# Kernel optimization log

Hardware: AMD Instinct MI355X
Metric: run time of the kernel (lower is better)

The kernel has to match this reference:

```python
import jax, jax.numpy as jnp
import numpy as np

K = 3
PAD = 1
EPS = 1e-5


def _unfold(x, k, pad):
    # torch.nn.Unfold(k, dilation=1, padding=pad, stride=1): output [B, C*k*k, L]
    # with channel-major ordering (c, ki, kj) in the second dim.
    B, C, H, W = x.shape
    xp = jnp.pad(x, ((0, 0), (0, 0), (pad, pad), (pad, pad)))
    Ho = H + 2 * pad - k + 1
    Wo = W + 2 * pad - k + 1
    patches = jnp.stack(
        [xp[:, :, i:i + Ho, j:j + Wo] for i in range(k) for j in range(k)],
        axis=2,
    )  # [B, C, k*k, Ho, Wo]
    return patches.reshape(B, C * k * k, Ho * Wo)


def _conv1x1(x, w, b):
    return jnp.einsum('bchw,oc->bohw', x, w) + b[None, :, None, None]


def _bn(x, g, b):
    # training-mode BatchNorm2d: batch stats over (B,H,W), biased variance
    mu = x.mean(axis=(0, 2, 3), keepdims=True)
    var = x.var(axis=(0, 2, 3), keepdims=True)
    return (x - mu) * jax.lax.rsqrt(var + EPS) * g[None, :, None, None] + b[None, :, None, None]


def _tri(x, w, b, g, be):
    return jax.nn.relu(_bn(_conv1x1(x, w, b), g, be))


def reference(x, w1, b1, g1, be1, w2, b2, g2, be2, wf, bf, gf, bef):
    B, C, H, W = x.shape
    k2 = K * K
    c = k2 // 2
    tri1 = _tri(x, w1, b1, g1, be1)  # key map  [B,C,H,W] (m=1)
    tri2 = _tri(x, w2, b2, g2, be2)  # query map
    # NOTE: faithful to source: plain row-major reshape of [B, C*k2, L] -> [B, C, L, k2]
    ku = _unfold(tri1, K, PAD).reshape(B, C, -1, k2)
    qu = _unfold(tri2, K, PAD).reshape(B, C, -1, k2)
    logits = ku * qu[..., c:c + 1] + ku[..., c:c + 1] * qu
    dl_weight = jax.nn.softmax(logits, axis=-1)[:, None]  # [B,1,C,L,k2]
    xu = _unfold(x, K, PAD).reshape(B, 1, C, -1, k2)       # m=1 -> [B,1,C,L,k2]
    # NOTE: faithful to source: row-major reshape to [B, C, k2, L], sum over axis -2
    pre = (dl_weight * xu).reshape(B, C, k2, -1).sum(axis=-2).reshape(B, C, H, W)
    return jax.nn.relu(_bn(_conv1x1(pre, wf, bf), gf, bef))


def setup_inputs() -> dict:
    key = jax.random.key(0)
    B, C, O, H, W = 4, 256, 256, 64, 64
    ks = jax.random.split(key, 4)
    s = 1.0 / np.sqrt(C)
    return {
        'x': jax.random.normal(ks[0], (B, C, H, W), dtype=jnp.float32),
        'w1': jax.random.normal(ks[1], (C, C), dtype=jnp.float32) * s,
        'b1': jnp.zeros((C,), jnp.float32),
        'g1': jnp.ones((C,), jnp.float32),
        'be1': jnp.zeros((C,), jnp.float32),
        'w2': jax.random.normal(ks[2], (C, C), dtype=jnp.float32) * s,
        'b2': jnp.zeros((C,), jnp.float32),
        'g2': jnp.ones((C,), jnp.float32),
        'be2': jnp.zeros((C,), jnp.float32),
        'wf': jax.random.normal(ks[3], (O, C), dtype=jnp.float32) * s,
        'bf': jnp.zeros((O,), jnp.float32),
        'gf': jnp.ones((O,), jnp.float32),
        'bef': jnp.zeros((O,), jnp.float32),
    }
```

## Files before the change

### kernel.cpp

```cpp
#include <hip/hip_runtime.h>

#define L 4096
#define CCH 256
#define NB 4
#define KP 40

typedef __attribute__((ext_vector_type(8))) short short8;
typedef __attribute__((ext_vector_type(4))) float f32x4;
typedef unsigned short ushort_t;

__device__ __forceinline__ unsigned short f2bf(float f) {
    unsigned u = __builtin_bit_cast(unsigned, f);
    u += 0x7FFF + ((u >> 16) & 1);
    return (unsigned short)(u >> 16);
}
__device__ __forceinline__ float bflo(unsigned w) {
    return __builtin_bit_cast(float, w << 16);
}
__device__ __forceinline__ float bfhi(unsigned w) {
    return __builtin_bit_cast(float, w & 0xFFFF0000u);
}

__global__ __launch_bounds__(256, 2) void dual_gemm_k(
    const float* __restrict__ x,
    const float* __restrict__ w1, const float* __restrict__ b1,
    const float* __restrict__ w2, const float* __restrict__ b2,
    ushort_t* __restrict__ y1, ushort_t* __restrict__ y2)
{
    __shared__ short sA1[128 * KP];
    __shared__ short sA2[128 * KP];
    __shared__ short sB [64 * KP];

    const int tid = threadIdx.x;
    const int l0 = blockIdx.x * 64;
    const int o0 = blockIdx.y * 128;
    const int b  = blockIdx.z;

    const int wv = tid >> 6;
    const int lane = tid & 63;
    const int m = lane & 15;
    const int quad = lane >> 4;

    const float* xb = x + (size_t)b * CCH * L;

    const int sl = tid & 63, soct = tid >> 6;
    const int sr = tid & 127, sh = tid >> 7;

    f32x4 acc1[2][4], acc2[2][4];
    #pragma unroll
    for (int io = 0; io < 2; ++io)
        #pragma unroll
        for (int jl = 0; jl < 4; ++jl) {
            acc1[io][jl] = (f32x4){0.f,0.f,0.f,0.f};
            acc2[io][jl] = (f32x4){0.f,0.f,0.f,0.f};
        }

    for (int s = 0; s < 8; ++s) {
        const int k0 = s * 32;
        __syncthreads();
        {
            const float* xs = xb + (size_t)(k0 + soct * 8) * L + l0 + sl;
            short8 v;
            #pragma unroll
            for (int j = 0; j < 8; ++j) v[j] = (short)f2bf(xs[(size_t)j * L]);
            *(short8*)&sB[sl * KP + soct * 8] = v;
        }
        {
            const float4* wp = (const float4*)&w1[(size_t)(o0 + sr) * CCH + k0 + sh * 16];
            float4 c0 = wp[0], c1 = wp[1], c2 = wp[2], c3 = wp[3];
            short8 p0 = {(short)f2bf(c0.x),(short)f2bf(c0.y),(short)f2bf(c0.z),(short)f2bf(c0.w),
                         (short)f2bf(c1.x),(short)f2bf(c1.y),(short)f2bf(c1.z),(short)f2bf(c1.w)};
            short8 p1 = {(short)f2bf(c2.x),(short)f2bf(c2.y),(short)f2bf(c2.z),(short)f2bf(c2.w),
                         (short)f2bf(c3.x),(short)f2bf(c3.y),(short)f2bf(c3.z),(short)f2bf(c3.w)};
            *(short8*)&sA1[sr * KP + sh * 16]     = p0;
            *(short8*)&sA1[sr * KP + sh * 16 + 8] = p1;
            const float4* wq = (const float4*)&w2[(size_t)(o0 + sr) * CCH + k0 + sh * 16];
            float4 d0 = wq[0], d1 = wq[1], d2 = wq[2], d3 = wq[3];
            short8 q0 = {(short)f2bf(d0.x),(short)f2bf(d0.y),(short)f2bf(d0.z),(short)f2bf(d0.w),
                         (short)f2bf(d1.x),(short)f2bf(d1.y),(short)f2bf(d1.z),(short)f2bf(d1.w)};
            short8 q1 = {(short)f2bf(d2.x),(short)f2bf(d2.y),(short)f2bf(d2.z),(short)f2bf(d2.w),
                         (short)f2bf(d3.x),(short)f2bf(d3.y),(short)f2bf(d3.z),(short)f2bf(d3.w)};
            *(short8*)&sA2[sr * KP + sh * 16]     = q0;
            *(short8*)&sA2[sr * KP + sh * 16 + 8] = q1;
        }
        __syncthreads();
        short8 a1[2], a2[2], bf[4];
        #pragma unroll
        for (int io = 0; io < 2; ++io) {
            a1[io] = *(const short8*)&sA1[(wv * 32 + io * 16 + m) * KP + quad * 8];
            a2[io] = *(const short8*)&sA2[(wv * 32 + io * 16 + m) * KP + quad * 8];
        }
        #pragma unroll
        for (int jl = 0; jl < 4; ++jl)
            bf[jl] = *(const short8*)&sB[(jl * 16 + m) * KP + quad * 8];
        #pragma unroll
        for (int io = 0; io < 2; ++io)
            #pragma unroll
            for (int jl = 0; jl < 4; ++jl) {
                acc1[io][jl] = __builtin_amdgcn_mfma_f32_16x16x32_bf16(a1[io], bf[jl], acc1[io][jl], 0, 0, 0);
                acc2[io][jl] = __builtin_amdgcn_mfma_f32_16x16x32_bf16(a2[io], bf[jl], acc2[io][jl], 0, 0, 0);
            }
    }

    #pragma unroll
    for (int io = 0; io < 2; ++io)
        #pragma unroll
        for (int reg = 0; reg < 4; ++reg) {
            const int o = o0 + wv * 32 + io * 16 + quad * 4 + reg;
            const float bb1 = b1[o], bb2 = b2[o];
            const size_t ro = ((size_t)b * CCH + o) * L + l0 + m;
            #pragma unroll
            for (int jl = 0; jl < 4; ++jl) {
                y1[ro + jl * 16] = f2bf(acc1[io][jl][reg] + bb1);
                y2[ro + jl * 16] = f2bf(acc2[io][jl][reg] + bb2);
            }
        }
}

__global__ __launch_bounds__(256, 2) void single_gemm_k(
    const ushort_t* __restrict__ x,
    const float* __restrict__ w, const float* __restrict__ bb,
    ushort_t* __restrict__ y)
{
    __shared__ short sA[128 * KP];
    __shared__ short sB[64 * KP];

    const int tid = threadIdx.x;
    const int l0 = blockIdx.x * 64;
    const int o0 = blockIdx.y * 128;
    const int b  = blockIdx.z;

    const int wv = tid >> 6;
    const int lane = tid & 63;
    const int m = lane & 15;
    const int quad = lane >> 4;

    const ushort_t* xb = x + (size_t)b * CCH * L;

    const int sl = tid & 63, soct = tid >> 6;
    const int sr = tid & 127, sh = tid >> 7;

    f32x4 acc[2][4];
    #pragma unroll
    for (int io = 0; io < 2; ++io)
        #pragma unroll
        for (int jl = 0; jl < 4; ++jl)
            acc[io][jl] = (f32x4){0.f,0.f,0.f,0.f};

    for (int s = 0; s < 8; ++s) {
        const int k0 = s * 32;
        __syncthreads();
        {
            const ushort_t* xs = xb + (size_t)(k0 + soct * 8) * L + l0 + sl;
            short8 v;
            #pragma unroll
            for (int j = 0; j < 8; ++j) v[j] = (short)xs[(size_t)j * L];
            *(short8*)&sB[sl * KP + soct * 8] = v;
        }
        {
            const float4* wp = (const float4*)&w[(size_t)(o0 + sr) * CCH + k0 + sh * 16];
            float4 c0 = wp[0], c1 = wp[1], c2 = wp[2], c3 = wp[3];
            short8 p0 = {(short)f2bf(c0.x),(short)f2bf(c0.y),(short)f2bf(c0.z),(short)f2bf(c0.w),
                         (short)f2bf(c1.x),(short)f2bf(c1.y),(short)f2bf(c1.z),(short)f2bf(c1.w)};
            short8 p1 = {(short)f2bf(c2.x),(short)f2bf(c2.y),(short)f2bf(c2.z),(short)f2bf(c2.w),
                         (short)f2bf(c3.x),(short)f2bf(c3.y),(short)f2bf(c3.z),(short)f2bf(c3.w)};
            *(short8*)&sA[sr * KP + sh * 16]     = p0;
            *(short8*)&sA[sr * KP + sh * 16 + 8] = p1;
        }
        __syncthreads();
        short8 a[2], bf[4];
        #pragma unroll
        for (int io = 0; io < 2; ++io)
            a[io] = *(const short8*)&sA[(wv * 32 + io * 16 + m) * KP + quad * 8];
        #pragma unroll
        for (int jl = 0; jl < 4; ++jl)
            bf[jl] = *(const short8*)&sB[(jl * 16 + m) * KP + quad * 8];
        #pragma unroll
        for (int io = 0; io < 2; ++io)
            #pragma unroll
            for (int jl = 0; jl < 4; ++jl)
                acc[io][jl] = __builtin_amdgcn_mfma_f32_16x16x32_bf16(a[io], bf[jl], acc[io][jl], 0, 0, 0);
    }

    #pragma unroll
    for (int io = 0; io < 2; ++io)
        #pragma unroll
        for (int reg = 0; reg < 4; ++reg) {
            const int o = o0 + wv * 32 + io * 16 + quad * 4 + reg;
            const float b0 = bb[o];
            const size_t ro = ((size_t)b * CCH + o) * L + l0 + m;
            #pragma unroll
            for (int jl = 0; jl < 4; ++jl)
                y[ro + jl * 16] = f2bf(acc[io][jl][reg] + b0);
        }
}

__device__ __forceinline__ void bn_stats_body(
    const ushort_t* y, const float* gamma, const float* beta,
    float* scale, float* shift, int c, int tid)
{
    float s = 0.f, s2 = 0.f;
    for (int b = 0; b < NB; ++b) {
        const uint4* p = (const uint4*)(y + ((size_t)b * CCH + c) * L);
        #pragma unroll
        for (int r = 0; r < 2; ++r) {
            uint4 v = p[r * 256 + tid];
            unsigned w[4] = {v.x, v.y, v.z, v.w};
            #pragma unroll
            for (int u = 0; u < 4; ++u) {
                float a = bflo(w[u]), bb = bfhi(w[u]);
                s  += a + bb;
                s2 += a * a + bb * bb;
            }
        }
    }
    #pragma unroll
    for (int off = 32; off > 0; off >>= 1) {
        s  += __shfl_down(s, off);
        s2 += __shfl_down(s2, off);
    }
    __shared__ float red[2][4];
    if ((tid & 63) == 0) { red[0][tid >> 6] = s; red[1][tid >> 6] = s2; }
    __syncthreads();
    if (tid == 0) {
        float S  = red[0][0] + red[0][1] + red[0][2] + red[0][3];
        float S2 = red[1][0] + red[1][1] + red[1][2] + red[1][3];
        const float invN = 1.f / (NB * (float)L);
        float mean = S * invN;
        float var  = S2 * invN - mean * mean;
        float rstd = rsqrtf(var + 1e-5f);
        float g = gamma[c];
        scale[c] = g * rstd;
        shift[c] = beta[c] - mean * g * rstd;
    }
}

__global__ __launch_bounds__(256) void bn_stats_k(
    const ushort_t* __restrict__ y, const float* __restrict__ gamma,
    const float* __restrict__ beta,
    float* __restrict__ scale, float* __restrict__ shift)
{
    bn_stats_body(y, gamma, beta, scale, shift, blockIdx.x, threadIdx.x);
}

__global__ __launch_bounds__(256) void bn_stats2_k(
    const ushort_t* __restrict__ y1, const float* __restrict__ g1, const float* __restrict__ be1,
    float* __restrict__ sc1, float* __restrict__ sh1,
    const ushort_t* __restrict__ y2, const float* __restrict__ g2, const float* __restrict__ be2,
    float* __restrict__ sc2, float* __restrict__ sh2)
{
    const int c = blockIdx.x & 255;
    if (blockIdx.x < 256) bn_stats_body(y1, g1, be1, sc1, sh1, c, threadIdx.x);
    else                  bn_stats_body(y2, g2, be2, sc2, sh2, c, threadIdx.x);
}

__global__ __launch_bounds__(512, 4) void attention_k(
    const float* __restrict__ x,
    const ushort_t* __restrict__ y1,
    const ushort_t* __restrict__ y2,
    const float* __restrict__ s1sc, const float* __restrict__ s1sh,
    const float* __restrict__ s2sc, const float* __restrict__ s2sh,
    ushort_t* __restrict__ pre)
{
    __shared__ unsigned sKQ[L];
    __shared__ float    sXv[L];
    __shared__ uint2    sCI[L];

    const int bc = blockIdx.x;
    const int tid = threadIdx.x;
    const int ch = bc & 255;
    const size_t off = (size_t)bc * L;

    const float sc1 = s1sc[ch], sh1 = s1sh[ch];
    const float sc2 = s2sc[ch], sh2 = s2sh[ch];

    const float4* x4 = (const float4*)(x + off);

    {
        uint4 ak = ((const uint4*)(y1 + off))[tid];
        uint4 aq = ((const uint4*)(y2 + off))[tid];
        unsigned wks[4] = {ak.x, ak.y, ak.z, ak.w};
        unsigned wqs[4] = {aq.x, aq.y, aq.z, aq.w};
        #pragma unroll
        for (int u = 0; u < 4; ++u) {
            float klo = fmaxf(fmaf(bflo(wks[u]), sc1, sh1), 0.f);
            float khi = fmaxf(fmaf(bfhi(wks[u]), sc1, sh1), 0.f);
            float qlo = fmaxf(fmaf(bflo(wqs[u]), sc2, sh2), 0.f);
            float qhi = fmaxf(fmaf(bfhi(wqs[u]), sc2, sh2), 0.f);
            sKQ[8 * tid + 2 * u]     = (unsigned)f2bf(klo) | ((unsigned)f2bf(qlo) << 16);
            sKQ[8 * tid + 2 * u + 1] = (unsigned)f2bf(khi) | ((unsigned)f2bf(qhi) << 16);
        }
        ((float4*)sXv)[2 * tid]     = x4[2 * tid];
        ((float4*)sXv)[2 * tid + 1] = x4[2 * tid + 1];
    }
    __syncthreads();

    #pragma unroll
    for (int r = 0; r < 8; ++r) {
        const int lp = r * 512 + tid;
        const int base = 9 * lp;
        float kv[9], qv[9];
        unsigned cw = 0;
        #pragma unroll
        for (int j = 0; j < 9; ++j) {
            int f = base + j;
            int t = f >> 12;
            int l = f & 4095;
            int di = (t * 86) >> 8;
            int dj = t - di * 3;
            int ii = (l >> 6) + di - 1;
            int jj = (l & 63) + dj - 1;
            bool ok = ((unsigned)ii < 64u) && ((unsigned)jj < 64u);
            int src = ((ii << 6) + jj) & 4095;
            unsigned w = sKQ[src];
            w = ok ? w : 0u;
            if (j == 4) cw = w;
            kv[j] = bflo(w);
            qv[j] = bfhi(w);
        }
        const float kc = kv[4], qc = qv[4];
        float s01 = __expf(kv[0] * qc + kc * qv[0]) + __expf(kv[1] * qc + kc * qv[1]);
        float s23 = __expf(kv[2] * qc + kc * qv[2]) + __expf(kv[3] * qc + kc * qv[3]);
        float s45 = __expf(kv[4] * qc + kc * qv[4]) + __expf(kv[5] * qc + kc * qv[5]);
        float s67 = __expf(kv[6] * qc + kc * qv[6]) + __expf(kv[7] * qc + kc * qv[7]);
        float s = ((s01 + s23) + (s45 + s67)) + __expf(kv[8] * qc + kc * qv[8]);
        uint2 ci;
        ci.x = cw;
        ci.y = __builtin_bit_cast(unsigned, -__logf(s));
        sCI[lp] = ci;
    }
    __syncthreads();

    #pragma unroll
    for (int r = 0; r < 8; ++r) {
        const int l = r * 512 + tid;
        const int li = l >> 6, lj = l & 63;
        float acc = 0.f;
        #pragma unroll
        for (int t = 0; t < 9; ++t) {
            const int f = (t << 12) + l;
            const unsigned lp = (unsigned)f / 9u;
            uint2 ci = sCI[lp];
            const float kc = bflo(ci.x), qc = bfhi(ci.x);
            const float cn = __builtin_bit_cast(float, ci.y);
            const int di = t / 3, dj = t % 3;
            int ii = li + di - 1;
            int jj = lj + dj - 1;
            bool ok = ((unsigned)ii < 64u) && ((unsigned)jj < 64u);
            int src = ((ii << 6) + jj) & 4095;
            unsigned w = sKQ[src];
            float xj = sXv[src];
            w  = ok ? w : 0u;
            xj = ok ? xj : 0.f;
            const float kj = bflo(w), qj = bfhi(w);
            float e = __expf(fmaf(kj, qc, fmaf(kc, qj, cn)));
            acc = fmaf(e, xj, acc);
        }
        pre[off + l] = f2bf(acc);
    }
}

__global__ __launch_bounds__(256) void bn_apply_k(
    const ushort_t* __restrict__ yf,
    const float* __restrict__ scale, const float* __restrict__ shift,
    float* __restrict__ out)
{
    const int i = blockIdx.x * 256 + threadIdx.x;
    const int ch = (i >> 9) & 255;
    const float sc = scale[ch], sh = shift[ch];

    uint4 v = ((const uint4*)yf)[i];
    unsigned w[4] = {v.x, v.y, v.z, v.w};
    float4 o0, o1;
    o0.x = fmaxf(fmaf(bflo(w[0]), sc, sh), 0.f);
    o0.y = fmaxf(fmaf(bfhi(w[0]), sc, sh), 0.f);
    o0.z = fmaxf(fmaf(bflo(w[1]), sc, sh), 0.f);
    o0.w = fmaxf(fmaf(bfhi(w[1]), sc, sh), 0.f);
    o1.x = fmaxf(fmaf(bflo(w[2]), sc, sh), 0.f);
    o1.y = fmaxf(fmaf(bfhi(w[2]), sc, sh), 0.f);
    o1.z = fmaxf(fmaf(bflo(w[3]), sc, sh), 0.f);
    o1.w = fmaxf(fmaf(bfhi(w[3]), sc, sh), 0.f);
    ((float4*)out)[2 * i]     = o0;
    ((float4*)out)[2 * i + 1] = o1;
}

extern "C" void kernel_launch(void* const* d_in, const int* in_sizes, int n_in,
                              void* d_out, int out_size, void* d_ws, size_t ws_size,
                              hipStream_t stream) {
    const float* x   = (const float*)d_in[0];
    const float* w1  = (const float*)d_in[1];
    const float* b1  = (const float*)d_in[2];
    const float* g1  = (const float*)d_in[3];
    const float* be1 = (const float*)d_in[4];
    const float* w2  = (const float*)d_in[5];
    const float* b2  = (const float*)d_in[6];
    const float* g2  = (const float*)d_in[7];
    const float* be2 = (const float*)d_in[8];
    const float* wf  = (const float*)d_in[9];
    const float* bf  = (const float*)d_in[10];
    const float* gf  = (const float*)d_in[11];
    const float* bef = (const float*)d_in[12];
    float* out = (float*)d_out;

    const size_t NEL = (size_t)NB * CCH * L;
    ushort_t* y1b = (ushort_t*)d_ws;
    ushort_t* y2b = y1b + NEL;
    float* st = (float*)(y2b + NEL);
    float* s1sc = st,        *s1sh = st + 256;
    float* s2sc = st + 512,  *s2sh = st + 768;
    float* sfsc = st + 1024, *sfsh = st + 1280;

    dim3 gg(64, 2, 4);
    dual_gemm_k<<<gg, 256, 0, stream>>>(x, w1, b1, w2, b2, y1b, y2b);
    bn_stats2_k<<<512, 256, 0, stream>>>(y1b, g1, be1, s1sc, s1sh,
                                         y2b, g2, be2, s2sc, s2sh);
    attention_k<<<NB * CCH, 512, 0, stream>>>(x, y1b, y2b,
                                              s1sc, s1sh, s2sc, s2sh,
                                              y2b);
    single_gemm_k<<<gg, 256, 0, stream>>>(y2b, wf, bf, y1b);
    bn_stats_k<<<256, 256, 0, stream>>>(y1b, gf, bef, sfsc, sfsh);
    bn_apply_k<<<(int)(NEL / 2048), 256, 0, stream>>>(y1b, sfsc, sfsh, out);
}
```

Measured before the change: 180.9 us.

## Use zero-padded shared tiles and bf16 x in attention kernel

The attention kernel now stores the key/query map and x in shared arrays with zero guard rows before and after the image. This removes per-tap row bounds checks and leaves only column-edge masks. x is stored as bf16 instead of fp32, which halves its LDS footprint and adds a rounding step to x. The first pass now reads contiguous 9-element runs with a specialized fast path. The second pass interchanges loops so each tap's offsets are computed once across eight accumulators. These changes aim to cut integer index arithmetic, LDS usage and predication, at the cost of extra precision loss on x.

```diff
diff --git a/kernel.cpp b/kernel.cpp
--- a/kernel.cpp
+++ b/kernel.cpp
@@ -4,6 +4,7 @@
 #define CCH 256
 #define NB 4
 #define KP 40
+#define GOF 72
 
 typedef __attribute__((ext_vector_type(8))) short short8;
 typedef __attribute__((ext_vector_type(4))) float f32x4;
@@ -19,6 +20,9 @@
 }
 __device__ __forceinline__ float bfhi(unsigned w) {
     return __builtin_bit_cast(float, w & 0xFFFF0000u);
+}
+__device__ __forceinline__ float bfu(ushort_t h) {
+    return __builtin_bit_cast(float, (unsigned)h << 16);
 }
 
 __global__ __launch_bounds__(256, 2) void dual_gemm_k(
@@ -262,9 +266,9 @@
     const float* __restrict__ s2sc, const float* __restrict__ s2sh,
     ushort_t* __restrict__ pre)
 {
-    __shared__ unsigned sKQ[L];
-    __shared__ float    sXv[L];
-    __shared__ uint2    sCI[L];
+    __shared__ unsigned sKQg[4240];
+    __shared__ ushort_t sXg [4240];
+    __shared__ uint2    sCI [L];
 
     const int bc = blockIdx.x;
     const int tid = threadIdx.x;
@@ -274,89 +278,118 @@
     const float sc1 = s1sc[ch], sh1 = s1sh[ch];
     const float sc2 = s2sc[ch], sh2 = s2sh[ch];
 
-    const float4* x4 = (const float4*)(x + off);
-
+    if (tid < GOF)  { sKQg[tid] = 0; sXg[tid] = 0; }
+    if (tid < 72)   { sKQg[GOF + 4096 + tid] = 0; sXg[GOF + 4096 + tid] = 0; }
     {
         uint4 ak = ((const uint4*)(y1 + off))[tid];
         uint4 aq = ((const uint4*)(y2 + off))[tid];
-        unsigned wks[4] = {ak.x, ak.y, ak.z, ak.w};
-        unsigned wqs[4] = {aq.x, aq.y, aq.z, aq.w};
+        float4 xa = ((const float4*)(x + off))[2 * tid];
+        float4 xb = ((const float4*)(x + off))[2 * tid + 1];
+        unsigned wk[4] = {ak.x, ak.y, ak.z, ak.w};
+        unsigned wq[4] = {aq.x, aq.y, aq.z, aq.w};
+        unsigned kq[8];
         #pragma unroll
         for (int u = 0; u < 4; ++u) {
-            float klo = fmaxf(fmaf(bflo(wks[u]), sc1, sh1), 0.f);
-            float khi = fmaxf(fmaf(bfhi(wks[u]), sc1, sh1), 0.f);
-            float qlo = fmaxf(fmaf(bflo(wqs[u]), sc2, sh2), 0.f);
-            float qhi = fmaxf(fmaf(bfhi(wqs[u]), sc2, sh2), 0.f);
-            sKQ[8 * tid + 2 * u]     = (unsigned)f2bf(klo) | ((unsigned)f2bf(qlo) << 16);
-            sKQ[8 * tid + 2 * u + 1] = (unsigned)f2bf(khi) | ((unsigned)f2bf(qhi) << 16);
-        }
-        ((float4*)sXv)[2 * tid]     = x4[2 * tid];
-        ((float4*)sXv)[2 * tid + 1] = x4[2 * tid + 1];
+            float klo = fmaxf(fmaf(bflo(wk[u]), sc1, sh1), 0.f);
+            float khi = fmaxf(fmaf(bfhi(wk[u]), sc1, sh1), 0.f);
+            float qlo = fmaxf(fmaf(bflo(wq[u]), sc2, sh2), 0.f);
+            float qhi = fmaxf(fmaf(bfhi(wq[u]), sc2, sh2), 0.f);
+            kq[2*u]   = (unsigned)f2bf(klo) | ((unsigned)f2bf(qlo) << 16);
+            kq[2*u+1] = (unsigned)f2bf(khi) | ((unsigned)f2bf(qhi) << 16);
+        }
+        *(uint4*)&sKQg[GOF + 8 * tid]     = make_uint4(kq[0], kq[1], kq[2], kq[3]);
+        *(uint4*)&sKQg[GOF + 8 * tid + 4] = make_uint4(kq[4], kq[5], kq[6], kq[7]);
+        float xv[8] = {xa.x, xa.y, xa.z, xa.w, xb.x, xb.y, xb.z, xb.w};
+        unsigned xp[4];
+        #pragma unroll
+        for (int u = 0; u < 4; ++u)
+            xp[u] = (unsigned)f2bf(xv[2*u]) | ((unsigned)f2bf(xv[2*u+1]) << 16);
+        *(uint4*)&sXg[GOF + 8 * tid] = make_uint4(xp[0], xp[1], xp[2], xp[3]);
     }
     __syncthreads();
 
-    #pragma unroll
-    for (int r = 0; r < 8; ++r) {
-        const int lp = r * 512 + tid;
-        const int base = 9 * lp;
-        float kv[9], qv[9];
-        unsigned cw = 0;
-        #pragma unroll
-        for (int j = 0; j < 9; ++j) {
-            int f = base + j;
-            int t = f >> 12;
-            int l = f & 4095;
-            int di = (t * 86) >> 8;
-            int dj = t - di * 3;
-            int ii = (l >> 6) + di - 1;
-            int jj = (l & 63) + dj - 1;
-            bool ok = ((unsigned)ii < 64u) && ((unsigned)jj < 64u);
-            int src = ((ii << 6) + jj) & 4095;
-            unsigned w = sKQ[src];
-            w = ok ? w : 0u;
-            if (j == 4) cw = w;
-            kv[j] = bflo(w);
-            qv[j] = bfhi(w);
-        }
-        const float kc = kv[4], qc = qv[4];
-        float s01 = __expf(kv[0] * qc + kc * qv[0]) + __expf(kv[1] * qc + kc * qv[1]);
-        float s23 = __expf(kv[2] * qc + kc * qv[2]) + __expf(kv[3] * qc + kc * qv[3]);
-        float s45 = __expf(kv[4] * qc + kc * qv[4]) + __expf(kv[5] * qc + kc * qv[5]);
-        float s67 = __expf(kv[6] * qc + kc * qv[6]) + __expf(kv[7] * qc + kc * qv[7]);
-        float s = ((s01 + s23) + (s45 + s67)) + __expf(kv[8] * qc + kc * qv[8]);
-        uint2 ci;
-        ci.x = cw;
-        ci.y = __builtin_bit_cast(unsigned, -__logf(s));
-        sCI[lp] = ci;
+    {
+        const int fbase = 9 * tid;
+        #pragma unroll
+        for (int r = 0; r < 8; ++r) {
+            const int f  = fbase + 4608 * r;
+            const int t  = f >> 12;
+            const int fl = f & 4095;
+            unsigned wv[9];
+            if (fl < 4088) {
+                const int di = (t * 86) >> 8;
+                const int dj = t - 3 * di;
+                const int cbad = (dj == 0) ? 0 : ((dj == 2) ? 63 : 99);
+                const int base = fl + (di << 6) + dj - 65 + GOF;
+                #pragma unroll
+                for (int j = 0; j < 9; ++j) wv[j] = sKQg[base + j];
+                #pragma unroll
+                for (int j = 0; j < 9; ++j) {
+                    int c = (fl + j) & 63;
+                    wv[j] = (c == cbad) ? 0u : wv[j];
+                }
+            } else {
+                #pragma unroll
+                for (int j = 0; j < 9; ++j) {
+                    int fj = f + j;
+                    int tj = fj >> 12, lj = fj & 4095;
+                    int dij = (tj * 86) >> 8, djj = tj - 3 * dij;
+                    int idx = lj + (dij << 6) + djj - 65 + GOF;
+                    unsigned wr = sKQg[idx];
+                    int c = lj & 63;
+                    int cb = (djj == 0) ? 0 : ((djj == 2) ? 63 : 99);
+                    wv[j] = (c == cb) ? 0u : wr;
+                }
+            }
+            const unsigned cw = wv[4];
+            const float kc = bflo(cw), qc = bfhi(cw);
+            float e0 = __expf(bflo(wv[0]) * qc + kc * bfhi(wv[0]));
+            float e1 = __expf(bflo(wv[1]) * qc + kc * bfhi(wv[1]));
+            float e2 = __expf(bflo(wv[2]) * qc + kc * bfhi(wv[2]));
+            float e3 = __expf(bflo(wv[3]) * qc + kc * bfhi(wv[3]));
+            float e4 = __expf(bflo(wv[4]) * qc + kc * bfhi(wv[4]));
+            float e5 = __expf(bflo(wv[5]) * qc + kc * bfhi(wv[5]));
+            float e6 = __expf(bflo(wv[6]) * qc + kc * bfhi(wv[6]));
+            float e7 = __expf(bflo(wv[7]) * qc + kc * bfhi(wv[7]));
+            float e8 = __expf(bflo(wv[8]) * qc + kc * bfhi(wv[8]));
+            float s = (((e0 + e1) + (e2 + e3)) + ((e4 + e5) + (e6 + e7))) + e8;
+            uint2 ci;
+            ci.x = cw;
+            ci.y = __builtin_bit_cast(unsigned, -__logf(s));
+            sCI[r * 512 + tid] = ci;
+        }
     }
     __syncthreads();
 
-    #pragma unroll
-    for (int r = 0; r < 8; ++r) {
-        const int l = r * 512 + tid;
-        const int li = l >> 6, lj = l & 63;
-        float acc = 0.f;
+    {
+        const int c0 = tid & 63;
+        float acc[8];
+        #pragma unroll
+        for (int r = 0; r < 8; ++r) acc[r] = 0.f;
+
         #pragma unroll
         for (int t = 0; t < 9; ++t) {
-            const int f = (t << 12) + l;
-            const unsigned lp = (unsigned)f / 9u;
-            uint2 ci = sCI[lp];
-            const float kc = bflo(ci.x), qc = bfhi(ci.x);
-            const float cn = __builtin_bit_cast(float, ci.y);
             const int di = t / 3, dj = t % 3;
-            int ii = li + di - 1;
-            int jj = lj + dj - 1;
-            bool ok = ((unsigned)ii < 64u) && ((unsigned)jj < 64u);
-            int src = ((ii << 6) + jj) & 4095;
-            unsigned w = sKQ[src];
-            float xj = sXv[src];
-            w  = ok ? w : 0u;
-            xj = ok ? xj : 0.f;
-            const float kj = bflo(w), qj = bfhi(w);
-            float e = __expf(fmaf(kj, qc, fmaf(kc, qj, cn)));
-            acc = fmaf(e, xj, acc);
-        }
-        pre[off + l] = f2bf(acc);
+            const int base = tid + (di << 6) + dj - 65 + GOF;
+            const bool colbad = (dj == 0) ? (c0 == 0) : ((dj == 2) ? (c0 == 63) : false);
+            const int ft = (t << 12) + tid;
+            #pragma unroll
+            for (int r = 0; r < 8; ++r) {
+                const int f = ft + 512 * r;
+                const unsigned lp = (unsigned)f / 9u;
+                uint2 ci = sCI[lp];
+                const float kc = bflo(ci.x), qc = bfhi(ci.x);
+                const float cn = __builtin_bit_cast(float, ci.y);
+                unsigned wv = sKQg[base + 512 * r];
+                float xj = bfu(sXg[base + 512 * r]);
+                xj = colbad ? 0.f : xj;
+                float e = __expf(fmaf(bflo(wv), qc, fmaf(kc, bfhi(wv), cn)));
+                acc[r] = fmaf(e, xj, acc[r]);
+            }
+        }
+        #pragma unroll
+        for (int r = 0; r < 8; ++r)
+            pre[off + r * 512 + tid] = f2bf(acc[r]);
     }
 }
 
```

Measured after the change: 171.2 us. -5.4%, faster.
